# Performance work log

Hardware: AMD Instinct MI355X
Metric: run time of the kernel (lower is better)

Reference implementation:

```python
import jax, jax.numpy as jnp
import numpy as np

B, S, V, K = 8, 128, 32000, 32


def setup_inputs() -> dict:
    key = jax.random.key(0)
    ks = jax.random.split(key, 8)
    return {
        "neural_logit": jax.random.normal(ks[0], (B, S, V), dtype=jnp.float32),
        "optor_vals": jax.random.randint(ks[1], (B, S, K), 0, V),
        "optor_dists": jax.random.uniform(ks[2], (B, S, K), dtype=jnp.float32) * 100.0,
        "const_vals": jax.random.randint(ks[3], (B, S, K), 0, V),
        "const_dists": jax.random.uniform(ks[4], (B, S, K), dtype=jnp.float32) * 100.0,
        "prev_words": jax.random.randint(ks[5], (B, S), 0, V),
        "optor_lamda": jnp.array([0.7], dtype=jnp.float32),
        "const_lamda": jnp.array([0.7], dtype=jnp.float32),
        "optor_temp": jnp.array([10.0], dtype=jnp.float32),
        "const_temp": jnp.array([10.0], dtype=jnp.float32),
    }


def _knn_prob(vals, dists, temp, vocab):
    # kernel-density: softmax over negative distances, scatter-add into vocab ids
    b, s, k = vals.shape
    w = jax.nn.softmax(-dists / temp, axis=-1)            # [B,S,K]
    rows = jnp.arange(b * s)[:, None]                     # [BS,1]
    p = jnp.zeros((b * s, vocab), w.dtype)
    p = p.at[rows, vals.reshape(b * s, k)].add(w.reshape(b * s, k))
    return p.reshape(b, s, vocab)


def reference(neural_logit, optor_vals, optor_dists, const_vals, const_dists,
              prev_words, optor_lamda, const_lamda, optor_temp, const_temp):
    nmt_prob = jax.nn.softmax(neural_logit, axis=-1)      # [B,S,V]

    optor_knn = _knn_prob(optor_vals, optor_dists, optor_temp[0], V)
    optor_combined = optor_lamda[0] * optor_knn + (1.0 - optor_lamda[0]) * nmt_prob

    const_knn = _knn_prob(const_vals, const_dists, const_temp[0], V)
    const_combined = const_lamda[0] * const_knn + (1.0 - const_lamda[0]) * nmt_prob

    pw = prev_words                                        # [B,S]
    optor_mask = (pw <= 88) | ((pw >= 91) & (pw <= 291))
    const_mask = (pw == 89) | (pw == 90) | (pw >= 292)

    combined = (optor_combined * optor_mask[:, :, None].astype(nmt_prob.dtype)
                + const_combined * const_mask[:, :, None].astype(nmt_prob.dtype))
    return combined
```

## Files before the change

kernel.cpp:

```cpp
#include <hip/hip_runtime.h>
#include <math.h>

constexpr int Bc = 8, Sc = 128, Vc = 32000, Kc = 32;
constexpr int NT = 1024;
constexpr int V4 = Vc / 4;
constexpr int ITERS = (V4 + NT - 1) / NT;
constexpr int NWAVES = NT / 64;

__global__ __launch_bounds__(NT) void SR_knnModel_kernel(
    const float* __restrict__ logit,
    const int*   __restrict__ optor_vals,
    const float* __restrict__ optor_dists,
    const int*   __restrict__ const_vals,
    const float* __restrict__ const_dists,
    const int*   __restrict__ prev_words,
    const float* __restrict__ optor_lamda,
    const float* __restrict__ const_lamda,
    const float* __restrict__ optor_temp,
    const float* __restrict__ const_temp,
    float* __restrict__ out)
{
    const int row = blockIdx.x;
    const int t   = threadIdx.x;
    const size_t base = (size_t)row * Vc;
    const float4* __restrict__ xin  = (const float4*)(logit + base);
    float4* __restrict__       xout = (float4*)(out + base);

    float4 r[ITERS];
    float lmax = -INFINITY;
#pragma unroll
    for (int i = 0; i < ITERS; ++i) {
        const int idx = t + i * NT;
        if (i < ITERS - 1 || idx < V4) {
            const float4 v = xin[idx];
            r[i] = v;
            lmax = fmaxf(lmax, fmaxf(fmaxf(v.x, v.y), fmaxf(v.z, v.w)));
        }
    }

    __shared__ float red[NWAVES];
#pragma unroll
    for (int off = 32; off > 0; off >>= 1)
        lmax = fmaxf(lmax, __shfl_xor(lmax, off));
    const int wave = t >> 6;
    if ((t & 63) == 0) red[wave] = lmax;
    __syncthreads();
    float bmax = red[0];
#pragma unroll
    for (int w = 1; w < NWAVES; ++w) bmax = fmaxf(bmax, red[w]);
    __syncthreads();

    float lsum = 0.f;
#pragma unroll
    for (int i = 0; i < ITERS; ++i) {
        const int idx = t + i * NT;
        if (i < ITERS - 1 || idx < V4) {
            float4 v = r[i];
            v.x = __expf(v.x - bmax);
            v.y = __expf(v.y - bmax);
            v.z = __expf(v.z - bmax);
            v.w = __expf(v.w - bmax);
            r[i] = v;
            lsum += (v.x + v.y) + (v.z + v.w);
        }
    }
#pragma unroll
    for (int off = 32; off > 0; off >>= 1)
        lsum += __shfl_xor(lsum, off);
    if ((t & 63) == 0) red[wave] = lsum;
    __syncthreads();
    float bsum = 0.f;
#pragma unroll
    for (int w = 0; w < NWAVES; ++w) bsum += red[w];

    const int pw = prev_words[row];
    const bool om = (pw <= 88) || (pw >= 91 && pw <= 291);
    const bool cm = (pw == 89) || (pw == 90) || (pw >= 292);
    const float omf = om ? 1.f : 0.f;
    const float cmf = cm ? 1.f : 0.f;
    const float ol = optor_lamda[0];
    const float cl = const_lamda[0];
    const float cn = (1.f - ol) * omf + (1.f - cl) * cmf;
    const float inv = cn / bsum;

#pragma unroll
    for (int i = 0; i < ITERS; ++i) {
        const int idx = t + i * NT;
        if (i < ITERS - 1 || idx < V4) {
            float4 v = r[i];
            v.x *= inv; v.y *= inv; v.z *= inv; v.w *= inv;
            xout[idx] = v;
        }
    }
    __syncthreads();

    if (t < 32 || (t >= 64 && t < 96)) {
        const bool is_opt = (t < 32);
        const float scale = is_opt ? ol * omf : cl * cmf;
        if (scale != 0.f) {
            const int k = t & 31;
            const int*   vals  = is_opt ? optor_vals  : const_vals;
            const float* dists = is_opt ? optor_dists : const_dists;
            const float  temp  = is_opt ? optor_temp[0] : const_temp[0];
            const float s = -dists[row * Kc + k] / temp;
            float m = s;
#pragma unroll
            for (int off = 16; off > 0; off >>= 1)
                m = fmaxf(m, __shfl_xor(m, off));
            const float e = __expf(s - m);
            float sm = e;
#pragma unroll
            for (int off = 16; off > 0; off >>= 1)
                sm += __shfl_xor(sm, off);
            const float w = e / sm;
            atomicAdd(out + base + vals[row * Kc + k], scale * w);
        }
    }
}

extern "C" void kernel_launch(void* const* d_in, const int* in_sizes, int n_in,
                              void* d_out, int out_size, void* d_ws, size_t ws_size,
                              hipStream_t stream) {
    const float* logit       = (const float*)d_in[0];
    const int*   optor_vals  = (const int*)  d_in[1];
    const float* optor_dists = (const float*)d_in[2];
    const int*   const_vals  = (const int*)  d_in[3];
    const float* const_dists = (const float*)d_in[4];
    const int*   prev_words  = (const int*)  d_in[5];
    const float* optor_lamda = (const float*)d_in[6];
    const float* const_lamda = (const float*)d_in[7];
    const float* optor_temp  = (const float*)d_in[8];
    const float* const_temp  = (const float*)d_in[9];
    float* out = (float*)d_out;

    SR_knnModel_kernel<<<Bc * Sc, NT, 0, stream>>>(
        logit, optor_vals, optor_dists, const_vals, const_dists, prev_words,
        optor_lamda, const_lamda, optor_temp, const_temp, out);
}
```

Before: 250.8 us.

## Split softmax into online-reduce, chunked map, and scatter kernels

Replaces the single register-resident 1024-thread-per-row kernel with three kernels. The first computes the row max and sum in one pass with an online softmax. The second re-reads the logits across 4 chunks per row and writes scaled exponentials with nontemporal stores. The third applies the kNN scatter-add. This aims to raise occupancy and parallelism, at the cost of reading the logits twice and adding two kernel launches.

New measurement: 271.0 us. 8.0% more time.

```diff
diff --git a/kernel.cpp b/kernel.cpp
--- a/kernel.cpp
+++ b/kernel.cpp
@@ -2,13 +2,93 @@
 #include <math.h>
 
 constexpr int Bc = 8, Sc = 128, Vc = 32000, Kc = 32;
-constexpr int NT = 1024;
+constexpr int ROWS = Bc * Sc;
 constexpr int V4 = Vc / 4;
-constexpr int ITERS = (V4 + NT - 1) / NT;
-constexpr int NWAVES = NT / 64;
+constexpr int NTA = 256;
+constexpr int NTB = 256;
+constexpr int CHUNKS = 4;
+constexpr int CHUNK_F4 = V4 / CHUNKS;
 
-__global__ __launch_bounds__(NT) void SR_knnModel_kernel(
+typedef float v4f __attribute__((ext_vector_type(4)));
+
+__global__ __launch_bounds__(NTA) void knn_reduce_kernel(
     const float* __restrict__ logit,
+    const int*   __restrict__ prev_words,
+    const float* __restrict__ optor_lamda,
+    const float* __restrict__ const_lamda,
+    float* __restrict__ ws)
+{
+    const int row = blockIdx.x;
+    const int t   = threadIdx.x;
+    const v4f* __restrict__ x = (const v4f*)(logit + (size_t)row * Vc);
+
+    float m = -INFINITY, s = 0.f;
+#pragma unroll 4
+    for (int i = t; i < V4; i += NTA) {
+        const v4f v = x[i];
+        const float m4 = fmaxf(fmaxf(v.x, v.y), fmaxf(v.z, v.w));
+        const float mn = fmaxf(m, m4);
+        s = s * __expf(m - mn)
+          + __expf(v.x - mn) + __expf(v.y - mn)
+          + __expf(v.z - mn) + __expf(v.w - mn);
+        m = mn;
+    }
+#pragma unroll
+    for (int off = 32; off > 0; off >>= 1) {
+        const float m2 = __shfl_xor(m, off);
+        const float s2 = __shfl_xor(s, off);
+        const float mn = fmaxf(m, m2);
+        s = s * __expf(m - mn) + s2 * __expf(m2 - mn);
+        m = mn;
+    }
+    __shared__ float rm[NTA / 64], rs[NTA / 64];
+    const int wave = t >> 6;
+    if ((t & 63) == 0) { rm[wave] = m; rs[wave] = s; }
+    __syncthreads();
+    if (t == 0) {
+        float M = rm[0];
+#pragma unroll
+        for (int w = 1; w < NTA / 64; ++w) M = fmaxf(M, rm[w]);
+        float Z = 0.f;
+#pragma unroll
+        for (int w = 0; w < NTA / 64; ++w) Z += rs[w] * __expf(rm[w] - M);
+
+        const int pw = prev_words[row];
+        const bool om = (pw <= 88) || (pw >= 91 && pw <= 291);
+        const bool cm = (pw == 89) || (pw == 90) || (pw >= 292);
+        const float cn = (1.f - optor_lamda[0]) * (om ? 1.f : 0.f)
+                       + (1.f - const_lamda[0]) * (cm ? 1.f : 0.f);
+        ws[2 * row]     = M;
+        ws[2 * row + 1] = cn / Z;
+    }
+}
+
+__global__ __launch_bounds__(NTB) void knn_map_kernel(
+    const float* __restrict__ logit,
+    const float* __restrict__ ws,
+    float* __restrict__ out)
+{
+    const int row = blockIdx.x;
+    const int t   = threadIdx.x;
+    const float M  = ws[2 * row];
+    const float sc = ws[2 * row + 1];
+    const size_t base4 = (size_t)row * V4;
+    const v4f* __restrict__ x = (const v4f*)logit + base4;
+    v4f* __restrict__       o = (v4f*)out + base4;
+    const int begin = blockIdx.y * CHUNK_F4;
+    const int end   = begin + CHUNK_F4;
+#pragma unroll 4
+    for (int i = begin + t; i < end; i += NTB) {
+        v4f v = x[i];
+        v.x = __expf(v.x - M) * sc;
+        v.y = __expf(v.y - M) * sc;
+        v.z = __expf(v.z - M) * sc;
+        v.w = __expf(v.w - M) * sc;
+        __builtin_nontemporal_store(v, &o[i]);
+    }
+}
+
+__global__ __launch_bounds__(64) void knn_scatter_kernel(
     const int*   __restrict__ optor_vals,
     const float* __restrict__ optor_dists,
     const int*   __restrict__ const_vals,
@@ -22,100 +102,33 @@
 {
     const int row = blockIdx.x;
     const int t   = threadIdx.x;
-    const size_t base = (size_t)row * Vc;
-    const float4* __restrict__ xin  = (const float4*)(logit + base);
-    float4* __restrict__       xout = (float4*)(out + base);
-
-    float4 r[ITERS];
-    float lmax = -INFINITY;
-#pragma unroll
-    for (int i = 0; i < ITERS; ++i) {
-        const int idx = t + i * NT;
-        if (i < ITERS - 1 || idx < V4) {
-            const float4 v = xin[idx];
-            r[i] = v;
-            lmax = fmaxf(lmax, fmaxf(fmaxf(v.x, v.y), fmaxf(v.z, v.w)));
-        }
-    }
-
-    __shared__ float red[NWAVES];
-#pragma unroll
-    for (int off = 32; off > 0; off >>= 1)
-        lmax = fmaxf(lmax, __shfl_xor(lmax, off));
-    const int wave = t >> 6;
-    if ((t & 63) == 0) red[wave] = lmax;
-    __syncthreads();
-    float bmax = red[0];
-#pragma unroll
-    for (int w = 1; w < NWAVES; ++w) bmax = fmaxf(bmax, red[w]);
-    __syncthreads();
-
-    float lsum = 0.f;
-#pragma unroll
-    for (int i = 0; i < ITERS; ++i) {
-        const int idx = t + i * NT;
-        if (i < ITERS - 1 || idx < V4) {
-            float4 v = r[i];
-            v.x = __expf(v.x - bmax);
-            v.y = __expf(v.y - bmax);
-            v.z = __expf(v.z - bmax);
-            v.w = __expf(v.w - bmax);
-            r[i] = v;
-            lsum += (v.x + v.y) + (v.z + v.w);
-        }
-    }
-#pragma unroll
-    for (int off = 32; off > 0; off >>= 1)
-        lsum += __shfl_xor(lsum, off);
-    if ((t & 63) == 0) red[wave] = lsum;
-    __syncthreads();
-    float bsum = 0.f;
-#pragma unroll
-    for (int w = 0; w < NWAVES; ++w) bsum += red[w];
+    const bool is_opt = (t < 32);
+    const int k = t & 31;
 
     const int pw = prev_words[row];
     const bool om = (pw <= 88) || (pw >= 91 && pw <= 291);
     const bool cm = (pw == 89) || (pw == 90) || (pw >= 292);
-    const float omf = om ? 1.f : 0.f;
-    const float cmf = cm ? 1.f : 0.f;
-    const float ol = optor_lamda[0];
-    const float cl = const_lamda[0];
-    const float cn = (1.f - ol) * omf + (1.f - cl) * cmf;
-    const float inv = cn / bsum;
+    const float scale = is_opt ? optor_lamda[0] * (om ? 1.f : 0.f)
+                               : const_lamda[0] * (cm ? 1.f : 0.f);
 
+    const int*   vals  = is_opt ? optor_vals  : const_vals;
+    const float* dists = is_opt ? optor_dists : const_dists;
+    const float  temp  = is_opt ? optor_temp[0] : const_temp[0];
+
+    const float sv = -dists[row * Kc + k] / temp;
+    float mx = sv;
 #pragma unroll
-    for (int i = 0; i < ITERS; ++i) {
-        const int idx = t + i * NT;
-        if (i < ITERS - 1 || idx < V4) {
-            float4 v = r[i];
-            v.x *= inv; v.y *= inv; v.z *= inv; v.w *= inv;
-            xout[idx] = v;
-        }
-    }
-    __syncthreads();
+    for (int off = 16; off > 0; off >>= 1)
+        mx = fmaxf(mx, __shfl_xor(mx, off));
+    const float e = __expf(sv - mx);
+    float sm = e;
+#pragma unroll
+    for (int off = 16; off > 0; off >>= 1)
+        sm += __shfl_xor(sm, off);
+    const float w = e / sm;
 
-    if (t < 32 || (t >= 64 && t < 96)) {
-        const bool is_opt = (t < 32);
-        const float scale = is_opt ? ol * omf : cl * cmf;
-        if (scale != 0.f) {
-            const int k = t & 31;
-            const int*   vals  = is_opt ? optor_vals  : const_vals;
-            const float* dists = is_opt ? optor_dists : const_dists;
-            const float  temp  = is_opt ? optor_temp[0] : const_temp[0];
-            const float s = -dists[row * Kc + k] / temp;
-            float m = s;
-#pragma unroll
-            for (int off = 16; off > 0; off >>= 1)
-                m = fmaxf(m, __shfl_xor(m, off));
-            const float e = __expf(s - m);
-            float sm = e;
-#pragma unroll
-            for (int off = 16; off > 0; off >>= 1)
-                sm += __shfl_xor(sm, off);
-            const float w = e / sm;
-            atomicAdd(out + base + vals[row * Kc + k], scale * w);
-        }
-    }
+    if (scale != 0.f)
+        atomicAdd(out + (size_t)row * Vc + vals[row * Kc + k], scale * w);
 }
 
 extern "C" void kernel_launch(void* const* d_in, const int* in_sizes, int n_in,
@@ -132,8 +145,14 @@
     const float* optor_temp  = (const float*)d_in[8];
     const float* const_temp  = (const float*)d_in[9];
     float* out = (float*)d_out;
+    float* ws  = (float*)d_ws;
 
-    SR_knnModel_kernel<<<Bc * Sc, NT, 0, stream>>>(
-        logit, optor_vals, optor_dists, const_vals, const_dists, prev_words,
+    knn_reduce_kernel<<<ROWS, NTA, 0, stream>>>(
+        logit, prev_words, optor_lamda, const_lamda, ws);
+
+    knn_map_kernel<<<dim3(ROWS, CHUNKS), NTB, 0, stream>>>(logit, ws, out);
+
+    knn_scatter_kernel<<<ROWS, 64, 0, stream>>>(
+        optor_vals, optor_dists, const_vals, const_dists, prev_words,
         optor_lamda, const_lamda, optor_temp, const_temp, out);
 }
```
